# Optimization experiments

Measured on AMD Instinct MI355X. Metric: run time of the kernel, lower is better.

## Reference

```python
import jax, jax.numpy as jnp
import numpy as np

B, S, H, E, D, K = 2, 4096, 1024, 8, 2048, 2


def setup_inputs() -> dict:
    key = jax.random.key(0)
    ks = jax.random.split(key, 6)
    scale = 0.02
    return {
        "x": jax.random.normal(ks[0], (B, S, H), dtype=jnp.float32),
        "gate_w": jax.random.normal(ks[1], (E, H), dtype=jnp.float32) * scale,
        "w1": jax.random.normal(ks[2], (E, H, D), dtype=jnp.float32) * scale,
        "b1": jnp.zeros((E, D), dtype=jnp.float32),
        "w2": jax.random.normal(ks[3], (E, D, H), dtype=jnp.float32) * scale,
        "b2": jnp.zeros((E, H), dtype=jnp.float32),
    }


def reference(x, gate_w, w1, b1, w2, b2):
    b, s, h = x.shape
    e = gate_w.shape[0]
    # Router
    router_logits = jnp.einsum('bsh,eh->bse', x, gate_w)
    router_probs = jax.nn.softmax(router_logits, axis=-1)
    top_k_probs, expert_idx = jax.lax.top_k(router_probs, K)      # [B,S,K]
    top_k_probs = top_k_probs / top_k_probs.sum(axis=-1, keepdims=True)
    # Aux load-balancing loss (faithful to source: mean over batch only -> [S,E])
    oh = jax.nn.one_hot(expert_idx, e, dtype=x.dtype)             # [B,S,K,E]
    tokens_per_expert = oh.sum(axis=-2).mean(axis=0)              # [S,E]
    avg_prob = router_probs.mean(axis=(0, 1))                     # [E]
    aux_loss = e * (tokens_per_expert * avg_prob).sum()
    # Dense combine weights per token per expert: [B*S, E]
    combine = (oh * top_k_probs[..., None]).sum(axis=-2).reshape(-1, e)
    # Expert MLPs, batched over experts (grouped GEMM form)
    xf = x.reshape(-1, h)                                         # [T,H]
    hid = jax.nn.gelu(jnp.einsum('th,ehd->etd', xf, w1) + b1[:, None, :],
                      approximate=False)                          # [E,T,D]
    y = jnp.einsum('etd,edh->eth', hid, w2) + b2[:, None, :]      # [E,T,H]
    out = jnp.einsum('te,eth->th', combine, y)                    # [T,H]
    return out.reshape(b, s, h), aux_loss
```

## Files before the change

### kernel.cpp

```cpp
#include <hip/hip_runtime.h>
#include <hip/hip_bf16.h>
#include <math.h>

#define Bdim 2
#define Sdim 4096
#define Hdim 1024
#define Edim 8
#define Ddim 2048
#define Tdim (Bdim*Sdim)

typedef __attribute__((ext_vector_type(8))) __bf16 bfv8;
typedef __attribute__((ext_vector_type(8))) short s16x8;
typedef __attribute__((ext_vector_type(4))) short s16x4;
typedef __attribute__((ext_vector_type(4))) float f32x4;

__device__ __forceinline__ short f2bf(float f) {
    union { float f; unsigned u; } a; a.f = f;
    unsigned r = (a.u + 0x7fffu + ((a.u >> 16) & 1u)) >> 16;
    return (short)r;
}
__device__ __forceinline__ float bf2f(short s) {
    union { unsigned u; float f; } a; a.u = ((unsigned)(unsigned short)s) << 16;
    return a.f;
}
__device__ __forceinline__ float fgelu(float x) {
    float u = fminf(x * (1.5957691f + 0.07135481f * x * x), 60.0f);
    float t = __expf(u);
    return x * t / (t + 1.0f);
}

typedef const __attribute__((address_space(1))) unsigned int ga_u32;
typedef __attribute__((address_space(3))) unsigned int la_u32;

__device__ __forceinline__ void gl_lds16(const void* g, void* l) {
    __builtin_amdgcn_global_load_lds((ga_u32*)g, (la_u32*)l, 16, 0, 0);
}

#define SYNC0() do {                                                     \
    asm volatile("s_waitcnt vmcnt(0)" ::: "memory");                     \
    __builtin_amdgcn_s_barrier();                                        \
    __builtin_amdgcn_sched_barrier(0);                                   \
} while (0)

#define RD1(S) do {                                                                  \
    _Pragma("unroll") for (int n = 0; n < 4; ++n)                                    \
        bf[n] = *(const bfv8*)(lds + 16384 + (S) * 8192 + offB[n]);                  \
    _Pragma("unroll") for (int m = 0; m < 8; ++m)                                    \
        af[m] = *(const bfv8*)(lds + (S) * 8192 + offA[m]);                          \
    __builtin_amdgcn_sched_barrier(0);                                               \
} while (0)
#define MM1() do {                                                                   \
    __builtin_amdgcn_s_setprio(1);                                                   \
    _Pragma("unroll") for (int m = 0; m < 8; ++m)                                    \
        _Pragma("unroll") for (int n = 0; n < 4; ++n)                                \
            acc[m][n] = __builtin_amdgcn_mfma_f32_16x16x32_bf16(af[m], bf[n], acc[m][n], 0, 0, 0); \
    __builtin_amdgcn_s_setprio(0);                                                   \
    __builtin_amdgcn_sched_barrier(0);                                               \
} while (0)
#define PH1F(SST, SRD) do { stage(SST); RD1(SRD); MM1(); SYNC0(); } while (0)
#define PH1L(SRD)      do { RD1(SRD); MM1(); } while (0)

#define RD2(S) do {                                                                  \
    _Pragma("unroll") for (int n = 0; n < 4; ++n)                                    \
        bf[n] = *(const bfv8*)(lds + 16384 + (S) * 4096 + offB[n]);                  \
    _Pragma("unroll") for (int m = 0; m < 4; ++m)                                    \
        af[m] = *(const bfv8*)(lds + (S) * 8192 + offA[m]);                          \
    __builtin_amdgcn_sched_barrier(0);                                               \
} while (0)
#define MM2() do {                                                                   \
    __builtin_amdgcn_s_setprio(1);                                                   \
    _Pragma("unroll") for (int m = 0; m < 4; ++m)                                    \
        _Pragma("unroll") for (int n = 0; n < 4; ++n)                                \
            acc[m][n] = __builtin_amdgcn_mfma_f32_16x16x32_bf16(af[m], bf[n], acc[m][n], 0, 0, 0); \
    __builtin_amdgcn_s_setprio(0);                                                   \
    __builtin_amdgcn_sched_barrier(0);                                               \
} while (0)
#define PH2F(SST, SRD) do { stage(SST); RD2(SRD); MM2(); SYNC0(); } while (0)
#define PH2L(SRD)      do { RD2(SRD); MM2(); } while (0)

__global__ __launch_bounds__(256) void router_kernel(
    const float* __restrict__ x, const float* __restrict__ gw,
    int* __restrict__ cnt, float* __restrict__ psum,
    int* __restrict__ ltok, float* __restrict__ lw,
    short* __restrict__ xb)
{
    __shared__ float gws[Edim * Hdim];
    __shared__ int   lcnt[Edim], gbase[Edim];
    __shared__ int   s_e[32], s_pos[32], s_tok[32];
    __shared__ float s_w[32];
    __shared__ float s_ps[4][8];

    int tid = threadIdx.x;
    for (int i = tid; i < Edim * Hdim / 4; i += 256)
        ((float4*)gws)[i] = ((const float4*)gw)[i];
    if (tid < Edim) lcnt[tid] = 0;
    __syncthreads();

    int wave = tid >> 6, lane = tid & 63;
    float ps = 0.f;

    for (int i = 0; i < 4; ++i) {
        int t = blockIdx.x * 16 + wave * 4 + i;
        double acc[Edim];
#pragma unroll
        for (int e = 0; e < Edim; ++e) acc[e] = 0.0;
#pragma unroll
        for (int kq = 0; kq < 4; ++kq) {
            float4 xv = *(const float4*)(x + (size_t)t * Hdim + kq * 256 + lane * 4);
            if (xb) {
                s16x4 h; h[0]=f2bf(xv.x); h[1]=f2bf(xv.y); h[2]=f2bf(xv.z); h[3]=f2bf(xv.w);
                *(s16x4*)(xb + (size_t)t * Hdim + kq * 256 + lane * 4) = h;
            }
#pragma unroll
            for (int e = 0; e < Edim; ++e) {
                float4 wv = *(const float4*)(&gws[e * Hdim + kq * 256 + lane * 4]);
                acc[e] += (double)xv.x * wv.x + (double)xv.y * wv.y
                        + (double)xv.z * wv.z + (double)xv.w * wv.w;
            }
        }
#pragma unroll
        for (int e = 0; e < Edim; ++e) {
            acc[e] += __shfl_xor(acc[e], 1, 64);
            acc[e] += __shfl_xor(acc[e], 2, 64);
            acc[e] += __shfl_xor(acc[e], 4, 64);
        }
        int el = lane & 7;
        double v = acc[0];
#pragma unroll
        for (int e = 1; e < Edim; ++e) if (el == e) v = acc[e];
        v += __shfl_xor(v, 8, 64);
        v += __shfl_xor(v, 16, 64);
        v += __shfl_xor(v, 32, 64);
        double mx = v;
        mx = fmax(mx, __shfl_xor(mx, 1, 64));
        mx = fmax(mx, __shfl_xor(mx, 2, 64));
        mx = fmax(mx, __shfl_xor(mx, 4, 64));
        float ex = __expf((float)(v - mx));
        float sm = ex;
        sm += __shfl_xor(sm, 1, 64);
        sm += __shfl_xor(sm, 2, 64);
        sm += __shfl_xor(sm, 4, 64);
        ps += ex / sm;
        double le[8];
#pragma unroll
        for (int e = 0; e < 8; ++e) le[e] = __shfl(v, e, 8);
        if (lane == 0) {
            int e1 = 0;
#pragma unroll
            for (int e = 1; e < 8; ++e) if (le[e] > le[e1]) e1 = e;
            int e2 = -1;
#pragma unroll
            for (int e = 0; e < 8; ++e) {
                if (e == e1) continue;
                if (e2 < 0 || le[e] > le[e2]) e2 = e;
            }
            float r = __expf((float)(le[e2] - le[e1]));
            float w1v = 1.0f / (1.0f + r);
            int lt = (wave * 4 + i) * 2;
            int p1 = atomicAdd(&lcnt[e1], 1);
            s_e[lt] = e1; s_pos[lt] = p1; s_tok[lt] = 2*t;     s_w[lt] = w1v;
            int p2 = atomicAdd(&lcnt[e2], 1);
            s_e[lt+1] = e2; s_pos[lt+1] = p2; s_tok[lt+1] = 2*t+1; s_w[lt+1] = 1.0f - w1v;
        }
    }
    if (lane < 8) s_ps[wave][lane] = ps;
    __syncthreads();
    if (tid < 8) {
        atomicAdd(&psum[tid], s_ps[0][tid] + s_ps[1][tid] + s_ps[2][tid] + s_ps[3][tid]);
        gbase[tid] = atomicAdd(&cnt[tid], lcnt[tid]);
    }
    __syncthreads();
    if (tid < 32) {
        int e = s_e[tid];
        int pos = gbase[e] + s_pos[tid];
        ltok[e * Tdim + pos] = s_tok[tid];
        lw[e * Tdim + pos] = s_w[tid];
    }
}

__global__ void aux_kernel(const int* __restrict__ cnt,
                           const float* __restrict__ psum,
                           int* __restrict__ eoff,
                           float* __restrict__ out_aux)
{
    if (threadIdx.x == 0 && blockIdx.x == 0) {
        double s = 0.0;
        int run = 0;
        for (int e = 0; e < Edim; ++e) {
            eoff[e] = run;
            run += cnt[e];
            s += ((double)cnt[e] / (double)Bdim) * ((double)psum[e] / (double)Tdim);
        }
        out_aux[0] = (float)((double)Edim * s);
    }
}

__global__ __launch_bounds__(256) void convt2_kernel(
    const float* __restrict__ w1, const float* __restrict__ w2,
    short* __restrict__ w1t, short* __restrict__ w2t)
{
    int z = blockIdx.z;
    const float* w; short* wt; int R, C, r0, c0, e;
    if (z < 8) { e = z;     w = w1; wt = w1t; R = Hdim; C = Ddim; r0 = blockIdx.y * 64; c0 = blockIdx.x * 64; }
    else       { e = z - 8; w = w2; wt = w2t; R = Ddim; C = Hdim; r0 = blockIdx.x * 64; c0 = blockIdx.y * 64; }

    __shared__ short t[64][76];
    int tid = threadIdx.x;
    {
        int r = tid >> 2, cs = (tid & 3) * 16;
        const float* src = w + ((size_t)e * R + r0 + r) * C + c0 + cs;
#pragma unroll
        for (int q = 0; q < 4; ++q) {
            float4 v = *(const float4*)(src + q * 4);
            s16x4 h; h[0]=f2bf(v.x); h[1]=f2bf(v.y); h[2]=f2bf(v.z); h[3]=f2bf(v.w);
            *(s16x4*)(&t[r][cs + q * 4]) = h;
        }
    }
    __syncthreads();
    {
        int c = tid >> 2, rs = (tid & 3) * 16;
        short tmp[16];
#pragma unroll
        for (int j = 0; j < 16; ++j) tmp[j] = t[rs + j][c];
        short* dst = wt + ((size_t)e * C + c0 + c) * R + r0 + rs;
        *(s16x8*)dst = *(s16x8*)tmp;
        *(s16x8*)(dst + 8) = *(s16x8*)(tmp + 8);
    }
}

__global__ __launch_bounds__(512, 2) void gemm1n_kernel(
    const short* __restrict__ xb, const short* __restrict__ w1t,
    const float* __restrict__ b1, const int* __restrict__ cnt,
    const int* __restrict__ eoff, const int* __restrict__ ltok,
    short* __restrict__ hid)
{
    constexpr int GXN = Ddim / 256;
    int id = blockIdx.x;
    int e = id & 7;
    unsigned rem = (unsigned)id >> 3;
    int bx = rem & (GXN - 1);
    int by = rem / GXN;

    int n_e = cnt[e];
    int row0 = by * 256;
    if (row0 >= n_e) return;
    int col0 = bx * 256;
    int slot0 = eoff[e];

    __shared__ short lds[32768];
    char* ldsb = (char*)lds;

    int tid = threadIdx.x;
    int w = tid >> 6, lane = tid & 63;

    const short* aS[2]; const short* bS[2];
    int oD[2];
#pragma unroll
    for (int j = 0; j < 2; ++j) {
        int o = tid * 16 + j * 8192;
        oD[j] = o;
        int eff = o ^ (((o >> 7) & 7) << 4);
        int row = ((eff >> 7) << 1) | ((eff >> 6) & 1);
        int kB  = eff & 63;
        int gr = row0 + row; if (gr > n_e - 1) gr = n_e - 1;
        int tok = ltok[(size_t)e * Tdim + gr] >> 1;
        aS[j] = xb + (size_t)tok * Hdim + (kB >> 1);
        bS[j] = w1t + ((size_t)e * Ddim + col0 + row) * Hdim + (kB >> 1);
    }

    int fr = lane & 15, kg = lane >> 4;
    int wm = (w >> 2) * 128, wn = (w & 3) * 64;

    int offA[8], offB[4];
#pragma unroll
    for (int m = 0; m < 8; ++m) {
        int r = wm + m * 16 + fr;
        offA[m] = (r >> 1) * 64 + ((((r & 1) * 32) + kg * 8) ^ (((r >> 1) & 7) << 3));
    }
#pragma unroll
    for (int n = 0; n < 4; ++n) {
        int r = wn + n * 16 + fr;
        offB[n] = (r >> 1) * 64 + ((((r & 1) * 32) + kg * 8) ^ (((r >> 1) & 7) << 3));
    }

    f32x4 acc[8][4];
#pragma unroll
    for (int m = 0; m < 8; ++m)
#pragma unroll
        for (int n = 0; n < 4; ++n) acc[m][n] = (f32x4)0.0f;

    bfv8 af[8], bf[4];

    auto stage = [&](int s) {
#pragma unroll
        for (int j = 0; j < 2; ++j) {
            gl_lds16(aS[j], ldsb + s * 16384 + oD[j]);
            aS[j] += 32;
            gl_lds16(bS[j], ldsb + 32768 + s * 16384 + oD[j]);
            bS[j] += 32;
        }
    };

    constexpr int NH = Hdim / 32;
    stage(0);
    SYNC0();
#pragma unroll 1
    for (int it = 0; it < (NH - 2) / 2; ++it) {
        PH1F(1, 0);
        PH1F(0, 1);
    }
    PH1F(1, 0);
    PH1L(1);

#pragma unroll
    for (int m = 0; m < 8; ++m) {
        int r0r = wm + m * 16 + kg * 4;
#pragma unroll
        for (int j = 0; j < 4; ++j) {
            int gr = row0 + r0r + j;
            if (gr >= n_e) continue;
            size_t hbase = (size_t)(slot0 + gr) * Ddim;
#pragma unroll
            for (int n = 0; n < 4; ++n) {
                int col = col0 + wn + n * 16 + fr;
                float v = acc[m][n][j] + b1[e * Ddim + col];
                hid[hbase + col] = f2bf(fgelu(v));
            }
        }
    }
}

__global__ __launch_bounds__(512, 2) void gemm2n_kernel(
    const short* __restrict__ hid, const short* __restrict__ w2t,
    const float* __restrict__ b2, const int* __restrict__ cnt,
    const int* __restrict__ eoff, const int* __restrict__ ltok,
    const float* __restrict__ lw, short* __restrict__ out2)
{
    constexpr int GXN = Hdim / 128;
    int id = blockIdx.x;
    int e = id & 7;
    unsigned rem = (unsigned)id >> 3;
    int bx = rem & (GXN - 1);
    int by = rem / GXN;

    int n_e = cnt[e];
    int row0 = by * 256;
    if (row0 >= n_e) return;
    int col0 = bx * 128;
    int slot0 = eoff[e];

    __shared__ short lds[24576];
    char* ldsb = (char*)lds;

    int tid = threadIdx.x;
    int w = tid >> 6, lane = tid & 63;

    const short* aS[2]; const short* bS0;
    int oD[2], oB;
#pragma unroll
    for (int j = 0; j < 2; ++j) {
        int o = tid * 16 + j * 8192;
        oD[j] = o;
        int eff = o ^ (((o >> 7) & 7) << 4);
        int row = ((eff >> 7) << 1) | ((eff >> 6) & 1);
        int kB  = eff & 63;
        int gr = row0 + row; if (gr > n_e - 1) gr = n_e - 1;
        aS[j] = hid + (size_t)(slot0 + gr) * Ddim + (kB >> 1);
    }
    {
        int o = tid * 16;
        oB = o;
        int eff = o ^ (((o >> 7) & 7) << 4);
        int row = ((eff >> 7) << 1) | ((eff >> 6) & 1);
        int kB  = eff & 63;
        bS0 = w2t + ((size_t)e * Hdim + col0 + row) * Ddim + (kB >> 1);
    }

    int fr = lane & 15, kg = lane >> 4;
    int wm = (w >> 1) * 64, wn = (w & 1) * 64;

    int offA[4], offB[4];
#pragma unroll
    for (int m = 0; m < 4; ++m) {
        int r = wm + m * 16 + fr;
        offA[m] = (r >> 1) * 64 + ((((r & 1) * 32) + kg * 8) ^ (((r >> 1) & 7) << 3));
    }
#pragma unroll
    for (int n = 0; n < 4; ++n) {
        int r = wn + n * 16 + fr;
        offB[n] = (r >> 1) * 64 + ((((r & 1) * 32) + kg * 8) ^ (((r >> 1) & 7) << 3));
    }

    f32x4 acc[4][4];
#pragma unroll
    for (int m = 0; m < 4; ++m)
#pragma unroll
        for (int n = 0; n < 4; ++n) acc[m][n] = (f32x4)0.0f;

    bfv8 af[4], bf[4];

    auto stage = [&](int s) {
#pragma unroll
        for (int j = 0; j < 2; ++j) {
            gl_lds16(aS[j], ldsb + s * 16384 + oD[j]);
            aS[j] += 32;
        }
        gl_lds16(bS0, ldsb + 32768 + s * 8192 + oB);
        bS0 += 32;
    };

    constexpr int NH = Ddim / 32;
    stage(0);
    SYNC0();
#pragma unroll 1
    for (int it = 0; it < (NH - 2) / 2; ++it) {
        PH2F(1, 0);
        PH2F(0, 1);
    }
    PH2F(1, 0);
    PH2L(1);

#pragma unroll
    for (int m = 0; m < 4; ++m) {
        int r0r = wm + m * 16 + kg * 4;
#pragma unroll
        for (int j = 0; j < 4; ++j) {
            int gr = row0 + r0r + j;
            if (gr >= n_e) continue;
            int val = ltok[(size_t)e * Tdim + gr];
            float p = lw[(size_t)e * Tdim + gr];
            size_t obase = (size_t)val * Hdim;
#pragma unroll
            for (int n = 0; n < 4; ++n) {
                int col = col0 + wn + n * 16 + fr;
                float v = p * (acc[m][n][j] + b2[e * Hdim + col]);
                out2[obase + col] = f2bf(v);
            }
        }
    }
}

__global__ __launch_bounds__(256) void combine_kernel(const short* __restrict__ out2,
                                                      float* __restrict__ out)
{
    size_t i = ((size_t)blockIdx.x * 256 + threadIdx.x) * 8;
    size_t t = i >> 10;
    int h = (int)(i & 1023);
    s16x8 a = *(const s16x8*)(out2 + (t * 2) * 1024 + h);
    s16x8 b = *(const s16x8*)(out2 + (t * 2 + 1) * 1024 + h);
    float4 o0, o1;
    o0.x = bf2f(a[0]) + bf2f(b[0]); o0.y = bf2f(a[1]) + bf2f(b[1]);
    o0.z = bf2f(a[2]) + bf2f(b[2]); o0.w = bf2f(a[3]) + bf2f(b[3]);
    o1.x = bf2f(a[4]) + bf2f(b[4]); o1.y = bf2f(a[5]) + bf2f(b[5]);
    o1.z = bf2f(a[6]) + bf2f(b[6]); o1.w = bf2f(a[7]) + bf2f(b[7]);
    *(float4*)(out + i) = o0;
    *(float4*)(out + i + 4) = o1;
}

#define FBK 64
#define FLDK 72

__global__ __launch_bounds__(256) void gemm1_fb(
    const float* __restrict__ x, const float* __restrict__ w1,
    const float* __restrict__ b1, const int* __restrict__ cnt,
    const int* __restrict__ ltok, short* __restrict__ hid,
    int CH, int row_base)
{
    int e = blockIdx.z;
    int n_e = cnt[e];
    int row0 = row_base + blockIdx.y * 128;
    if (row0 >= n_e) return;
    int col0 = blockIdx.x * 128;

    __shared__ short As[128][FLDK];
    __shared__ short Bs[128][FLDK];

    int tid = threadIdx.x;
    int arow = tid >> 1;
    int akh  = (tid & 1) * 32;
    int gr_a = row0 + arow;
    int tok = ltok[(size_t)e * Tdim + (gr_a < n_e ? gr_a : n_e - 1)] >> 1;
    const float* xrow = x + (size_t)tok * Hdim + akh;
    int bdg = (tid & 31) * 4;
    int bkg = (tid >> 5) * 4;

    int lane = tid & 63;
    int wid = tid >> 6;
    int wm = (wid >> 1) * 64, wn = (wid & 1) * 64;
    int fr = lane & 15, kg = lane >> 4;

    f32x4 acc[4][4];
#pragma unroll
    for (int m = 0; m < 4; ++m)
#pragma unroll
        for (int n = 0; n < 4; ++n) acc[m][n] = (f32x4)0.0f;

    const float* wB = w1 + (size_t)e * Hdim * Ddim + col0;

    for (int k0 = 0; k0 < Hdim; k0 += FBK) {
#pragma unroll
        for (int i = 0; i < 8; ++i) {
            float4 v = *(const float4*)(xrow + k0 + i * 4);
            s16x4 h; h[0] = f2bf(v.x); h[1] = f2bf(v.y); h[2] = f2bf(v.z); h[3] = f2bf(v.w);
            *(s16x4*)(&As[arow][akh + i * 4]) = h;
        }
#pragma unroll
        for (int r = 0; r < 2; ++r) {
            int kq = bkg + r * 32;
            float4 v0 = *(const float4*)(wB + (size_t)(k0 + kq + 0) * Ddim + bdg);
            float4 v1 = *(const float4*)(wB + (size_t)(k0 + kq + 1) * Ddim + bdg);
            float4 v2 = *(const float4*)(wB + (size_t)(k0 + kq + 2) * Ddim + bdg);
            float4 v3 = *(const float4*)(wB + (size_t)(k0 + kq + 3) * Ddim + bdg);
            const float* p0 = (const float*)&v0; const float* p1 = (const float*)&v1;
            const float* p2 = (const float*)&v2; const float* p3 = (const float*)&v3;
#pragma unroll
            for (int c = 0; c < 4; ++c) {
                s16x4 h; h[0] = f2bf(p0[c]); h[1] = f2bf(p1[c]); h[2] = f2bf(p2[c]); h[3] = f2bf(p3[c]);
                *(s16x4*)(&Bs[bdg + c][kq]) = h;
            }
        }
        __syncthreads();
        bfv8 af[4][2], bfr[4][2];
#pragma unroll
        for (int m = 0; m < 4; ++m)
#pragma unroll
            for (int kk = 0; kk < 2; ++kk)
                af[m][kk] = *(const bfv8*)(&As[wm + m * 16 + fr][kk * 32 + kg * 8]);
#pragma unroll
        for (int n = 0; n < 4; ++n)
#pragma unroll
            for (int kk = 0; kk < 2; ++kk)
                bfr[n][kk] = *(const bfv8*)(&Bs[wn + n * 16 + fr][kk * 32 + kg * 8]);
#pragma unroll
        for (int m = 0; m < 4; ++m)
#pragma unroll
            for (int n = 0; n < 4; ++n) {
                acc[m][n] = __builtin_amdgcn_mfma_f32_16x16x32_bf16(af[m][0], bfr[n][0], acc[m][n], 0, 0, 0);
                acc[m][n] = __builtin_amdgcn_mfma_f32_16x16x32_bf16(af[m][1], bfr[n][1], acc[m][n], 0, 0, 0);
            }
        __syncthreads();
    }

    int lr0 = row0 - row_base;
#pragma unroll
    for (int m = 0; m < 4; ++m) {
        int r0r = wm + m * 16 + kg * 4;
#pragma unroll
        for (int j = 0; j < 4; ++j) {
            int gr = row0 + r0r + j;
            if (gr >= n_e) continue;
            size_t hbase = ((size_t)e * CH + (size_t)(lr0 + r0r + j)) * Ddim;
#pragma unroll
            for (int n = 0; n < 4; ++n) {
                int col = col0 + wn + n * 16 + fr;
                float v = acc[m][n][j] + b1[e * Ddim + col];
                float g = 0.5f * v * (1.0f + erff(v * 0.70710678118654752440f));
                hid[hbase + col] = f2bf(g);
            }
        }
    }
}

__global__ __launch_bounds__(256) void gemm2_fb(
    const short* __restrict__ hid, const float* __restrict__ w2,
    const float* __restrict__ b2, const int* __restrict__ cnt,
    const int* __restrict__ ltok, const float* __restrict__ lw,
    float* __restrict__ out, int CH, int row_base)
{
    int e = blockIdx.z;
    int n_e = cnt[e];
    int row0 = row_base + blockIdx.y * 128;
    if (row0 >= n_e) return;
    int col0 = blockIdx.x * 128;

    __shared__ short As[128][FLDK];
    __shared__ short Bs[128][FLDK];

    int tid = threadIdx.x;
    int arow = tid >> 1;
    int akh  = (tid & 1) * 32;
    const short* hrow = hid + ((size_t)e * CH + (size_t)(row0 - row_base + arow)) * Ddim + akh;
    int bdg = (tid & 31) * 4;
    int bkg = (tid >> 5) * 4;

    int lane = tid & 63;
    int wid = tid >> 6;
    int wm = (wid >> 1) * 64, wn = (wid & 1) * 64;
    int fr = lane & 15, kg = lane >> 4;

    f32x4 acc[4][4];
#pragma unroll
    for (int m = 0; m < 4; ++m)
#pragma unroll
        for (int n = 0; n < 4; ++n) acc[m][n] = (f32x4)0.0f;

    const float* wB = w2 + (size_t)e * Ddim * Hdim + col0;

    for (int k0 = 0; k0 < Ddim; k0 += FBK) {
#pragma unroll
        for (int i = 0; i < 4; ++i) {
            s16x8 v = *(const s16x8*)(hrow + k0 + i * 8);
            *(s16x8*)(&As[arow][akh + i * 8]) = v;
        }
#pragma unroll
        for (int r = 0; r < 2; ++r) {
            int kq = bkg + r * 32;
            float4 v0 = *(const float4*)(wB + (size_t)(k0 + kq + 0) * Hdim + bdg);
            float4 v1 = *(const float4*)(wB + (size_t)(k0 + kq + 1) * Hdim + bdg);
            float4 v2 = *(const float4*)(wB + (size_t)(k0 + kq + 2) * Hdim + bdg);
            float4 v3 = *(const float4*)(wB + (size_t)(k0 + kq + 3) * Hdim + bdg);
            const float* p0 = (const float*)&v0; const float* p1 = (const float*)&v1;
            const float* p2 = (const float*)&v2; const float* p3 = (const float*)&v3;
#pragma unroll
            for (int c = 0; c < 4; ++c) {
                s16x4 h; h[0] = f2bf(p0[c]); h[1] = f2bf(p1[c]); h[2] = f2bf(p2[c]); h[3] = f2bf(p3[c]);
                *(s16x4*)(&Bs[bdg + c][kq]) = h;
            }
        }
        __syncthreads();
        bfv8 af[4][2], bfr[4][2];
#pragma unroll
        for (int m = 0; m < 4; ++m)
#pragma unroll
            for (int kk = 0; kk < 2; ++kk)
                af[m][kk] = *(const bfv8*)(&As[wm + m * 16 + fr][kk * 32 + kg * 8]);
#pragma unroll
        for (int n = 0; n < 4; ++n)
#pragma unroll
            for (int kk = 0; kk < 2; ++kk)
                bfr[n][kk] = *(const bfv8*)(&Bs[wn + n * 16 + fr][kk * 32 + kg * 8]);
#pragma unroll
        for (int m = 0; m < 4; ++m)
#pragma unroll
            for (int n = 0; n < 4; ++n) {
                acc[m][n] = __builtin_amdgcn_mfma_f32_16x16x32_bf16(af[m][0], bfr[n][0], acc[m][n], 0, 0, 0);
                acc[m][n] = __builtin_amdgcn_mfma_f32_16x16x32_bf16(af[m][1], bfr[n][1], acc[m][n], 0, 0, 0);
            }
        __syncthreads();
    }

#pragma unroll
    for (int m = 0; m < 4; ++m) {
        int r0r = wm + m * 16 + kg * 4;
#pragma unroll
        for (int j = 0; j < 4; ++j) {
            int gr = row0 + r0r + j;
            if (gr >= n_e) continue;
            int tok = ltok[(size_t)e * Tdim + gr] >> 1;
            float p = lw[(size_t)e * Tdim + gr];
#pragma unroll
            for (int n = 0; n < 4; ++n) {
                int col = col0 + wn + n * 16 + fr;
                float v = p * (acc[m][n][j] + b2[e * Hdim + col]);
                atomicAdd(&out[(size_t)tok * Hdim + col], v);
            }
        }
    }
}

extern "C" void kernel_launch(void* const* d_in, const int* in_sizes, int n_in,
                              void* d_out, int out_size, void* d_ws, size_t ws_size,
                              hipStream_t stream)
{
    const float* x  = (const float*)d_in[0];
    const float* gw = (const float*)d_in[1];
    const float* w1 = (const float*)d_in[2];
    const float* b1 = (const float*)d_in[3];
    const float* w2 = (const float*)d_in[4];
    const float* b2 = (const float*)d_in[5];
    float* out = (float*)d_out;

    char* wsb = (char*)d_ws;
    int*   cnt  = (int*)wsb;
    float* psum = (float*)(wsb + 32);
    int*   eoff = (int*)(wsb + 64);
    int*   ltok = (int*)(wsb + 128);
    float* lwp  = (float*)(wsb + 128 + (size_t)Edim * Tdim * 4);
    size_t lists_end = 128 + (size_t)Edim * Tdim * 8;

    size_t xb_sz = (size_t)Tdim * Hdim * 2;
    size_t w1t_sz = (size_t)Edim * Hdim * Ddim * 2;
    size_t w2t_sz = w1t_sz;
    size_t hid_sz = (size_t)(2 * Tdim) * Ddim * 2;
    size_t req = lists_end + xb_sz + w1t_sz + w2t_sz + hid_sz;

    hipMemsetAsync(wsb, 0, 128, stream);

    if (req <= ws_size) {
        short* xb   = (short*)(wsb + lists_end);
        short* w1t  = (short*)(wsb + lists_end + xb_sz);
        short* w2t  = (short*)(wsb + lists_end + xb_sz + w1t_sz);
        short* hid  = (short*)(wsb + lists_end + xb_sz + w1t_sz + w2t_sz);
        short* out2 = w1t;

        convt2_kernel<<<dim3(32, 16, 16), 256, 0, stream>>>(w1, w2, w1t, w2t);
        router_kernel<<<Tdim / 16, 256, 0, stream>>>(x, gw, cnt, psum, ltok, lwp, xb);
        aux_kernel<<<1, 64, 0, stream>>>(cnt, psum, eoff, out + (size_t)Tdim * Hdim);

        gemm1n_kernel<<<(Ddim / 256) * 32 * Edim, 512, 0, stream>>>(
            xb, w1t, b1, cnt, eoff, ltok, hid);
        gemm2n_kernel<<<(Hdim / 128) * 32 * Edim, 512, 0, stream>>>(
            hid, w2t, b2, cnt, eoff, ltok, lwp, out2);
        combine_kernel<<<(size_t)Tdim * Hdim / 2048, 256, 0, stream>>>(out2, out);
    } else {
        short* hid = (short*)(wsb + lists_end);
        int CH2 = 2048;
        while (CH2 > 128 && lists_end + (size_t)Edim * CH2 * Ddim * 2 > ws_size) CH2 >>= 1;

        hipMemsetAsync(d_out, 0, (size_t)out_size * 4, stream);
        router_kernel<<<Tdim / 16, 256, 0, stream>>>(x, gw, cnt, psum, ltok, lwp, nullptr);
        aux_kernel<<<1, 64, 0, stream>>>(cnt, psum, eoff, out + (size_t)Tdim * Hdim);

        int chunks = Tdim / CH2;
        for (int c = 0; c < chunks; ++c) {
            gemm1_fb<<<dim3(Ddim / 128, CH2 / 128, Edim), 256, 0, stream>>>(
                x, w1, b1, cnt, ltok, hid, CH2, c * CH2);
            gemm2_fb<<<dim3(Hdim / 128, CH2 / 128, Edim), 256, 0, stream>>>(
                hid, w2, b2, cnt, ltok, lwp, out, CH2, c * CH2);
        }
    }
}
```

Baseline: 327.4 us.

## Fuse router with weight conversion and scatter-add GEMM2 output atomically

Merges the weight transpose/convert kernel and the router kernel into one launch, with blocks split by index and shared memory held in a union. GEMM2 now does fp32 atomicAdd straight into the zeroed output instead of writing a bf16 intermediate per expert slot, so the separate combine kernel is gone. This removes one launch and a bf16 round trip through memory, at the cost of a full output memset and roughly 16M global float atomics, which may contend. Summation order is no longer fixed, so results can vary slightly between runs.

```diff
diff --git a/kernel.cpp b/kernel.cpp
--- a/kernel.cpp
+++ b/kernel.cpp
@@ -78,103 +78,139 @@
 #define PH2F(SST, SRD) do { stage(SST); RD2(SRD); MM2(); SYNC0(); } while (0)
 #define PH2L(SRD)      do { RD2(SRD); MM2(); } while (0)
 
-__global__ __launch_bounds__(256) void router_kernel(
+union PrepSm {
+    struct {
+        float gws[Edim * Hdim];
+        int lcnt[8], gbase[8];
+        int s_e[32], s_pos[32], s_tok[32];
+        float s_w[32];
+        float s_ps[4][8];
+    } r;
+    struct { short t[64][76]; } c;
+};
+
+__global__ __launch_bounds__(256) void prep_kernel(
     const float* __restrict__ x, const float* __restrict__ gw,
+    const float* __restrict__ w1, const float* __restrict__ w2,
     int* __restrict__ cnt, float* __restrict__ psum,
     int* __restrict__ ltok, float* __restrict__ lw,
-    short* __restrict__ xb)
+    short* __restrict__ xb, short* __restrict__ w1t, short* __restrict__ w2t)
 {
-    __shared__ float gws[Edim * Hdim];
-    __shared__ int   lcnt[Edim], gbase[Edim];
-    __shared__ int   s_e[32], s_pos[32], s_tok[32];
-    __shared__ float s_w[32];
-    __shared__ float s_ps[4][8];
-
+    __shared__ PrepSm sm;
     int tid = threadIdx.x;
-    for (int i = tid; i < Edim * Hdim / 4; i += 256)
-        ((float4*)gws)[i] = ((const float4*)gw)[i];
-    if (tid < Edim) lcnt[tid] = 0;
-    __syncthreads();
-
-    int wave = tid >> 6, lane = tid & 63;
-    float ps = 0.f;
-
-    for (int i = 0; i < 4; ++i) {
-        int t = blockIdx.x * 16 + wave * 4 + i;
-        double acc[Edim];
-#pragma unroll
-        for (int e = 0; e < Edim; ++e) acc[e] = 0.0;
-#pragma unroll
-        for (int kq = 0; kq < 4; ++kq) {
-            float4 xv = *(const float4*)(x + (size_t)t * Hdim + kq * 256 + lane * 4);
-            if (xb) {
+
+    if (blockIdx.x < Tdim / 16) {
+        int bid = blockIdx.x;
+        for (int i = tid; i < Edim * Hdim / 4; i += 256)
+            ((float4*)sm.r.gws)[i] = ((const float4*)gw)[i];
+        if (tid < Edim) sm.r.lcnt[tid] = 0;
+        __syncthreads();
+
+        int wave = tid >> 6, lane = tid & 63;
+        float ps = 0.f;
+
+        for (int i = 0; i < 4; ++i) {
+            int t = bid * 16 + wave * 4 + i;
+            double acc[Edim];
+#pragma unroll
+            for (int e = 0; e < Edim; ++e) acc[e] = 0.0;
+#pragma unroll
+            for (int kq = 0; kq < 4; ++kq) {
+                float4 xv = *(const float4*)(x + (size_t)t * Hdim + kq * 256 + lane * 4);
                 s16x4 h; h[0]=f2bf(xv.x); h[1]=f2bf(xv.y); h[2]=f2bf(xv.z); h[3]=f2bf(xv.w);
                 *(s16x4*)(xb + (size_t)t * Hdim + kq * 256 + lane * 4) = h;
+#pragma unroll
+                for (int e = 0; e < Edim; ++e) {
+                    float4 wv = *(const float4*)(&sm.r.gws[e * Hdim + kq * 256 + lane * 4]);
+                    acc[e] += (double)xv.x * wv.x + (double)xv.y * wv.y
+                            + (double)xv.z * wv.z + (double)xv.w * wv.w;
+                }
             }
 #pragma unroll
             for (int e = 0; e < Edim; ++e) {
-                float4 wv = *(const float4*)(&gws[e * Hdim + kq * 256 + lane * 4]);
-                acc[e] += (double)xv.x * wv.x + (double)xv.y * wv.y
-                        + (double)xv.z * wv.z + (double)xv.w * wv.w;
-            }
-        }
-#pragma unroll
-        for (int e = 0; e < Edim; ++e) {
-            acc[e] += __shfl_xor(acc[e], 1, 64);
-            acc[e] += __shfl_xor(acc[e], 2, 64);
-            acc[e] += __shfl_xor(acc[e], 4, 64);
-        }
-        int el = lane & 7;
-        double v = acc[0];
-#pragma unroll
-        for (int e = 1; e < Edim; ++e) if (el == e) v = acc[e];
-        v += __shfl_xor(v, 8, 64);
-        v += __shfl_xor(v, 16, 64);
-        v += __shfl_xor(v, 32, 64);
-        double mx = v;
-        mx = fmax(mx, __shfl_xor(mx, 1, 64));
-        mx = fmax(mx, __shfl_xor(mx, 2, 64));
-        mx = fmax(mx, __shfl_xor(mx, 4, 64));
-        float ex = __expf((float)(v - mx));
-        float sm = ex;
-        sm += __shfl_xor(sm, 1, 64);
-        sm += __shfl_xor(sm, 2, 64);
-        sm += __shfl_xor(sm, 4, 64);
-        ps += ex / sm;
-        double le[8];
-#pragma unroll
-        for (int e = 0; e < 8; ++e) le[e] = __shfl(v, e, 8);
-        if (lane == 0) {
-            int e1 = 0;
-#pragma unroll
-            for (int e = 1; e < 8; ++e) if (le[e] > le[e1]) e1 = e;
-            int e2 = -1;
-#pragma unroll
-            for (int e = 0; e < 8; ++e) {
-                if (e == e1) continue;
-                if (e2 < 0 || le[e] > le[e2]) e2 = e;
-            }
-            float r = __expf((float)(le[e2] - le[e1]));
-            float w1v = 1.0f / (1.0f + r);
-            int lt = (wave * 4 + i) * 2;
-            int p1 = atomicAdd(&lcnt[e1], 1);
-            s_e[lt] = e1; s_pos[lt] = p1; s_tok[lt] = 2*t;     s_w[lt] = w1v;
-            int p2 = atomicAdd(&lcnt[e2], 1);
-            s_e[lt+1] = e2; s_pos[lt+1] = p2; s_tok[lt+1] = 2*t+1; s_w[lt+1] = 1.0f - w1v;
-        }
-    }
-    if (lane < 8) s_ps[wave][lane] = ps;
-    __syncthreads();
-    if (tid < 8) {
-        atomicAdd(&psum[tid], s_ps[0][tid] + s_ps[1][tid] + s_ps[2][tid] + s_ps[3][tid]);
-        gbase[tid] = atomicAdd(&cnt[tid], lcnt[tid]);
-    }
-    __syncthreads();
-    if (tid < 32) {
-        int e = s_e[tid];
-        int pos = gbase[e] + s_pos[tid];
-        ltok[e * Tdim + pos] = s_tok[tid];
-        lw[e * Tdim + pos] = s_w[tid];
+                acc[e] += __shfl_xor(acc[e], 1, 64);
+                acc[e] += __shfl_xor(acc[e], 2, 64);
+                acc[e] += __shfl_xor(acc[e], 4, 64);
+            }
+            int el = lane & 7;
+            double v = acc[0];
+#pragma unroll
+            for (int e = 1; e < Edim; ++e) if (el == e) v = acc[e];
+            v += __shfl_xor(v, 8, 64);
+            v += __shfl_xor(v, 16, 64);
+            v += __shfl_xor(v, 32, 64);
+            double mx = v;
+            mx = fmax(mx, __shfl_xor(mx, 1, 64));
+            mx = fmax(mx, __shfl_xor(mx, 2, 64));
+            mx = fmax(mx, __shfl_xor(mx, 4, 64));
+            float ex = __expf((float)(v - mx));
+            float smv = ex;
+            smv += __shfl_xor(smv, 1, 64);
+            smv += __shfl_xor(smv, 2, 64);
+            smv += __shfl_xor(smv, 4, 64);
+            ps += ex / smv;
+            double le[8];
+#pragma unroll
+            for (int e = 0; e < 8; ++e) le[e] = __shfl(v, e, 8);
+            if (lane == 0) {
+                int e1 = 0;
+#pragma unroll
+                for (int e = 1; e < 8; ++e) if (le[e] > le[e1]) e1 = e;
+                int e2 = -1;
+#pragma unroll
+                for (int e = 0; e < 8; ++e) {
+                    if (e == e1) continue;
+                    if (e2 < 0 || le[e] > le[e2]) e2 = e;
+                }
+                float r = __expf((float)(le[e2] - le[e1]));
+                float w1v = 1.0f / (1.0f + r);
+                int lt = (wave * 4 + i) * 2;
+                int p1 = atomicAdd(&sm.r.lcnt[e1], 1);
+                sm.r.s_e[lt] = e1; sm.r.s_pos[lt] = p1; sm.r.s_tok[lt] = 2*t;     sm.r.s_w[lt] = w1v;
+                int p2 = atomicAdd(&sm.r.lcnt[e2], 1);
+                sm.r.s_e[lt+1] = e2; sm.r.s_pos[lt+1] = p2; sm.r.s_tok[lt+1] = 2*t+1; sm.r.s_w[lt+1] = 1.0f - w1v;
+            }
+        }
+        if (lane < 8) sm.r.s_ps[wave][lane] = ps;
+        __syncthreads();
+        if (tid < 8) {
+            atomicAdd(&psum[tid], sm.r.s_ps[0][tid] + sm.r.s_ps[1][tid] + sm.r.s_ps[2][tid] + sm.r.s_ps[3][tid]);
+            sm.r.gbase[tid] = atomicAdd(&cnt[tid], sm.r.lcnt[tid]);
+        }
+        __syncthreads();
+        if (tid < 32) {
+            int e = sm.r.s_e[tid];
+            int pos = sm.r.gbase[e] + sm.r.s_pos[tid];
+            ltok[e * Tdim + pos] = sm.r.s_tok[tid];
+            lw[e * Tdim + pos] = sm.r.s_w[tid];
+        }
+    } else {
+        int id = blockIdx.x - Tdim / 16;
+        int bz = id >> 9, by = (id >> 5) & 15, bx = id & 31;
+        const float* w; short* wt; int R, C, r0, c0, e;
+        if (bz < 8) { e = bz;     w = w1; wt = w1t; R = Hdim; C = Ddim; r0 = by * 64; c0 = bx * 64; }
+        else        { e = bz - 8; w = w2; wt = w2t; R = Ddim; C = Hdim; r0 = bx * 64; c0 = by * 64; }
+
+        {
+            int r = tid >> 2, cs = (tid & 3) * 16;
+            const float* src = w + ((size_t)e * R + r0 + r) * C + c0 + cs;
+#pragma unroll
+            for (int q = 0; q < 4; ++q) {
+                float4 v = *(const float4*)(src + q * 4);
+                s16x4 h; h[0]=f2bf(v.x); h[1]=f2bf(v.y); h[2]=f2bf(v.z); h[3]=f2bf(v.w);
+                *(s16x4*)(&sm.c.t[r][cs + q * 4]) = h;
+            }
+        }
+        __syncthreads();
+        {
+            int c = tid >> 2, rs = (tid & 3) * 16;
+            short tmp[16];
+#pragma unroll
+            for (int j = 0; j < 16; ++j) tmp[j] = sm.c.t[rs + j][c];
+            short* dst = wt + ((size_t)e * C + c0 + c) * R + r0 + rs;
+            *(s16x8*)dst = *(s16x8*)tmp;
+            *(s16x8*)(dst + 8) = *(s16x8*)(tmp + 8);
+        }
     }
 }
 
@@ -195,36 +231,98 @@
     }
 }
 
-__global__ __launch_bounds__(256) void convt2_kernel(
-    const float* __restrict__ w1, const float* __restrict__ w2,
-    short* __restrict__ w1t, short* __restrict__ w2t)
+__global__ __launch_bounds__(256) void router_kernel(
+    const float* __restrict__ x, const float* __restrict__ gw,
+    int* __restrict__ cnt, float* __restrict__ psum,
+    int* __restrict__ ltok, float* __restrict__ lw)
 {
-    int z = blockIdx.z;
-    const float* w; short* wt; int R, C, r0, c0, e;
-    if (z < 8) { e = z;     w = w1; wt = w1t; R = Hdim; C = Ddim; r0 = blockIdx.y * 64; c0 = blockIdx.x * 64; }
-    else       { e = z - 8; w = w2; wt = w2t; R = Ddim; C = Hdim; r0 = blockIdx.x * 64; c0 = blockIdx.y * 64; }
-
-    __shared__ short t[64][76];
+    __shared__ float gws[Edim * Hdim];
+    __shared__ int   lcnt[Edim], gbase[Edim];
+    __shared__ int   s_e[32], s_pos[32], s_tok[32];
+    __shared__ float s_w[32];
+    __shared__ float s_ps[4][8];
+
     int tid = threadIdx.x;
-    {
-        int r = tid >> 2, cs = (tid & 3) * 16;
-        const float* src = w + ((size_t)e * R + r0 + r) * C + c0 + cs;
-#pragma unroll
-        for (int q = 0; q < 4; ++q) {
-            float4 v = *(const float4*)(src + q * 4);
-            s16x4 h; h[0]=f2bf(v.x); h[1]=f2bf(v.y); h[2]=f2bf(v.z); h[3]=f2bf(v.w);
-            *(s16x4*)(&t[r][cs + q * 4]) = h;
-        }
-    }
+    for (int i = tid; i < Edim * Hdim / 4; i += 256)
+        ((float4*)gws)[i] = ((const float4*)gw)[i];
+    if (tid < Edim) lcnt[tid] = 0;
     __syncthreads();
-    {
-        int c = tid >> 2, rs = (tid & 3) * 16;
-        short tmp[16];
-#pragma unroll
-        for (int j = 0; j < 16; ++j) tmp[j] = t[rs + j][c];
-        short* dst = wt + ((size_t)e * C + c0 + c) * R + r0 + rs;
-        *(s16x8*)dst = *(s16x8*)tmp;
-        *(s16x8*)(dst + 8) = *(s16x8*)(tmp + 8);
+
+    int wave = tid >> 6, lane = tid & 63;
+    float ps = 0.f;
+
+    for (int i = 0; i < 4; ++i) {
+        int t = blockIdx.x * 16 + wave * 4 + i;
+        double acc[Edim];
+#pragma unroll
+        for (int e = 0; e < Edim; ++e) acc[e] = 0.0;
+#pragma unroll
+        for (int kq = 0; kq < 4; ++kq) {
+            float4 xv = *(const float4*)(x + (size_t)t * Hdim + kq * 256 + lane * 4);
+#pragma unroll
+            for (int e = 0; e < Edim; ++e) {
+                float4 wv = *(const float4*)(&gws[e * Hdim + kq * 256 + lane * 4]);
+                acc[e] += (double)xv.x * wv.x + (double)xv.y * wv.y
+                        + (double)xv.z * wv.z + (double)xv.w * wv.w;
+            }
+        }
+#pragma unroll
+        for (int e = 0; e < Edim; ++e) {
+            acc[e] += __shfl_xor(acc[e], 1, 64);
+            acc[e] += __shfl_xor(acc[e], 2, 64);
+            acc[e] += __shfl_xor(acc[e], 4, 64);
+        }
+        int el = lane & 7;
+        double v = acc[0];
+#pragma unroll
+        for (int e = 1; e < Edim; ++e) if (el == e) v = acc[e];
+        v += __shfl_xor(v, 8, 64);
+        v += __shfl_xor(v, 16, 64);
+        v += __shfl_xor(v, 32, 64);
+        double mx = v;
+        mx = fmax(mx, __shfl_xor(mx, 1, 64));
+        mx = fmax(mx, __shfl_xor(mx, 2, 64));
+        mx = fmax(mx, __shfl_xor(mx, 4, 64));
+        float ex = __expf((float)(v - mx));
+        float smv = ex;
+        smv += __shfl_xor(smv, 1, 64);
+        smv += __shfl_xor(smv, 2, 64);
+        smv += __shfl_xor(smv, 4, 64);
+        ps += ex / smv;
+        double le[8];
+#pragma unroll
+        for (int e = 0; e < 8; ++e) le[e] = __shfl(v, e, 8);
+        if (lane == 0) {
+            int e1 = 0;
+#pragma unroll
+            for (int e = 1; e < 8; ++e) if (le[e] > le[e1]) e1 = e;
+            int e2 = -1;
+#pragma unroll
+            for (int e = 0; e < 8; ++e) {
+                if (e == e1) continue;
+                if (e2 < 0 || le[e] > le[e2]) e2 = e;
+            }
+            float r = __expf((float)(le[e2] - le[e1]));
+            float w1v = 1.0f / (1.0f + r);
+            int lt = (wave * 4 + i) * 2;
+            int p1 = atomicAdd(&lcnt[e1], 1);
+            s_e[lt] = e1; s_pos[lt] = p1; s_tok[lt] = 2*t;     s_w[lt] = w1v;
+            int p2 = atomicAdd(&lcnt[e2], 1);
+            s_e[lt+1] = e2; s_pos[lt+1] = p2; s_tok[lt+1] = 2*t+1; s_w[lt+1] = 1.0f - w1v;
+        }
+    }
+    if (lane < 8) s_ps[wave][lane] = ps;
+    __syncthreads();
+    if (tid < 8) {
+        atomicAdd(&psum[tid], s_ps[0][tid] + s_ps[1][tid] + s_ps[2][tid] + s_ps[3][tid]);
+        gbase[tid] = atomicAdd(&cnt[tid], lcnt[tid]);
+    }
+    __syncthreads();
+    if (tid < 32) {
+        int e = s_e[tid];
+        int pos = gbase[e] + s_pos[tid];
+        ltok[e * Tdim + pos] = s_tok[tid];
+        lw[e * Tdim + pos] = s_w[tid];
     }
 }
 
@@ -334,7 +432,7 @@
     const short* __restrict__ hid, const short* __restrict__ w2t,
     const float* __restrict__ b2, const int* __restrict__ cnt,
     const int* __restrict__ eoff, const int* __restrict__ ltok,
-    const float* __restrict__ lw, short* __restrict__ out2)
+    const float* __restrict__ lw, float* __restrict__ out)
 {
     constexpr int GXN = Hdim / 128;
     int id = blockIdx.x;
@@ -427,34 +525,17 @@
         for (int j = 0; j < 4; ++j) {
             int gr = row0 + r0r + j;
             if (gr >= n_e) continue;
-            int val = ltok[(size_t)e * Tdim + gr];
+            int tok = ltok[(size_t)e * Tdim + gr] >> 1;
             float p = lw[(size_t)e * Tdim + gr];
-            size_t obase = (size_t)val * Hdim;
+            size_t obase = (size_t)tok * Hdim;
 #pragma unroll
             for (int n = 0; n < 4; ++n) {
                 int col = col0 + wn + n * 16 + fr;
                 float v = p * (acc[m][n][j] + b2[e * Hdim + col]);
-                out2[obase + col] = f2bf(v);
-            }
-        }
-    }
-}
-
-__global__ __launch_bounds__(256) void combine_kernel(const short* __restrict__ out2,
-                                                      float* __restrict__ out)
-{
-    size_t i = ((size_t)blockIdx.x * 256 + threadIdx.x) * 8;
-    size_t t = i >> 10;
-    int h = (int)(i & 1023);
-    s16x8 a = *(const s16x8*)(out2 + (t * 2) * 1024 + h);
-    s16x8 b = *(const s16x8*)(out2 + (t * 2 + 1) * 1024 + h);
-    float4 o0, o1;
-    o0.x = bf2f(a[0]) + bf2f(b[0]); o0.y = bf2f(a[1]) + bf2f(b[1]);
-    o0.z = bf2f(a[2]) + bf2f(b[2]); o0.w = bf2f(a[3]) + bf2f(b[3]);
-    o1.x = bf2f(a[4]) + bf2f(b[4]); o1.y = bf2f(a[5]) + bf2f(b[5]);
-    o1.z = bf2f(a[6]) + bf2f(b[6]); o1.w = bf2f(a[7]) + bf2f(b[7]);
-    *(float4*)(out + i) = o0;
-    *(float4*)(out + i + 4) = o1;
+                atomicAdd(&out[obase + col], v);
+            }
+        }
+    }
 }
 
 #define FBK 64
@@ -685,30 +766,28 @@
     size_t req = lists_end + xb_sz + w1t_sz + w2t_sz + hid_sz;
 
     hipMemsetAsync(wsb, 0, 128, stream);
+    hipMemsetAsync(d_out, 0, (size_t)out_size * 4, stream);
 
     if (req <= ws_size) {
         short* xb   = (short*)(wsb + lists_end);
         short* w1t  = (short*)(wsb + lists_end + xb_sz);
         short* w2t  = (short*)(wsb + lists_end + xb_sz + w1t_sz);
         short* hid  = (short*)(wsb + lists_end + xb_sz + w1t_sz + w2t_sz);
-        short* out2 = w1t;
-
-        convt2_kernel<<<dim3(32, 16, 16), 256, 0, stream>>>(w1, w2, w1t, w2t);
-        router_kernel<<<Tdim / 16, 256, 0, stream>>>(x, gw, cnt, psum, ltok, lwp, xb);
+
+        prep_kernel<<<Tdim / 16 + 8192, 256, 0, stream>>>(
+            x, gw, w1, w2, cnt, psum, ltok, lwp, xb, w1t, w2t);
         aux_kernel<<<1, 64, 0, stream>>>(cnt, psum, eoff, out + (size_t)Tdim * Hdim);
 
         gemm1n_kernel<<<(Ddim / 256) * 32 * Edim, 512, 0, stream>>>(
             xb, w1t, b1, cnt, eoff, ltok, hid);
         gemm2n_kernel<<<(Hdim / 128) * 32 * Edim, 512, 0, stream>>>(
-            hid, w2t, b2, cnt, eoff, ltok, lwp, out2);
-        combine_kernel<<<(size_t)Tdim * Hdim / 2048, 256, 0, stream>>>(out2, out);
+            hid, w2t, b2, cnt, eoff, ltok, lwp, out);
     } else {
         short* hid = (short*)(wsb + lists_end);
         int CH2 = 2048;
         while (CH2 > 128 && lists_end + (size_t)Edim * CH2 * Ddim * 2 > ws_size) CH2 >>= 1;
 
-        hipMemsetAsync(d_out, 0, (size_t)out_size * 4, stream);
-        router_kernel<<<Tdim / 16, 256, 0, stream>>>(x, gw, cnt, psum, ltok, lwp, nullptr);
+        router_kernel<<<Tdim / 16, 256, 0, stream>>>(x, gw, cnt, psum, ltok, lwp);
         aux_kernel<<<1, 64, 0, stream>>>(cnt, psum, eoff, out + (size_t)Tdim * Hdim);
 
         int chunks = Tdim / CH2;
```

After: 392.1 us. 1.2x slower.
